# Kernel tuning notes

Hardware: AMD Instinct MI355X
Metric: run time of the kernel (lower is better)

## Reference

```python
import jax, jax.numpy as jnp
import numpy as np

B, C, G, S, R = 8192, 4096, 16, 256, 512  # batch, in_channels, clusters, cluster_size, j_rank


def setup_inputs() -> dict:
    key = jax.random.key(0)
    kx, kw, kb, kp = jax.random.split(key, 4)
    x = jax.random.normal(kx, (B, C), dtype=jnp.float32)
    # per-cluster Linear weights [G, out=R, in=S] and biases [G, R]
    W = jax.random.normal(kw, (G, R, S), dtype=jnp.float32) * (1.0 / np.sqrt(S))
    b = jax.random.normal(kb, (G, R), dtype=jnp.float32) * 0.01
    # arrangements: non-contiguous channel clusters = random permutation split into G groups
    perm = jax.random.permutation(kp, C).reshape(G, S).astype(jnp.int32)
    return {"x": x, "W": W, "b": b, "perm": perm}


def reference(x, W, b, perm):
    # gather each cluster's channels: [B, G, S]
    xg = x[:, perm]
    # batched per-cluster linear (y = x_c @ W_c^T + b_c), then concat along dim 1
    out = jnp.einsum('bgs,grs->bgr', xg, W) + b  # [B, G, R]
    return out.reshape(x.shape[0], G * R)
```

## Files before the change

### kernel.cpp

```cpp
#include <hip/hip_runtime.h>

#define BB 8192
#define CC 4096
#define GG 16
#define SS 256
#define RR 512
#define NN (GG*RR)

typedef __bf16 bf16x8 __attribute__((ext_vector_type(8)));
typedef float  f32x4_t __attribute__((ext_vector_type(4)));

__device__ __forceinline__ unsigned short f2bf(float f){
  union{float f; unsigned int u;} v; v.f = f;
  unsigned int r = (v.u + 0x7FFFu + ((v.u>>16)&1u)) >> 16;
  return (unsigned short)r;
}

__device__ __forceinline__ void gld_lds16(const void* g, void* l){
  __builtin_amdgcn_global_load_lds((const __attribute__((address_space(1))) void*)g,
                                   (__attribute__((address_space(3))) void*)l, 16, 0, 0);
}

__global__ void __launch_bounds__(256) prep_kernel(
    const float* __restrict__ x, const int* __restrict__ perm,
    const float* __restrict__ W,
    unsigned short* __restrict__ xp, unsigned short* __restrict__ Wb)
{
  __shared__ float row[CC];
  const int tid = threadIdx.x;
  const int bid = blockIdx.x;
  if (bid < BB) {
    const size_t b = bid;
    const float4* xr = (const float4*)(x + b*CC);
    float4* rr = (float4*)row;
    #pragma unroll
    for (int c=0;c<4;++c) rr[c*256+tid] = xr[c*256+tid];
    __syncthreads();
    unsigned short* xo = xp + b*CC;
    #pragma unroll
    for (int c=0;c<2;++c){
      const int j0 = (((c<<8)+tid)<<3);
      const int* pp = perm + j0;
      unsigned int w0 = (unsigned)f2bf(row[pp[0]]) | ((unsigned)f2bf(row[pp[1]])<<16);
      unsigned int w1 = (unsigned)f2bf(row[pp[2]]) | ((unsigned)f2bf(row[pp[3]])<<16);
      unsigned int w2 = (unsigned)f2bf(row[pp[4]]) | ((unsigned)f2bf(row[pp[5]])<<16);
      unsigned int w3 = (unsigned)f2bf(row[pp[6]]) | ((unsigned)f2bf(row[pp[7]])<<16);
      uint4 o; o.x=w0; o.y=w1; o.z=w2; o.w=w3;
      *(uint4*)(xo + j0) = o;
    }
  } else {
    const int i = (((bid - BB)<<8) + tid)<<3;
    float4 f0 = ((const float4*)(W+i))[0];
    float4 f1 = ((const float4*)(W+i))[1];
    uint4 o;
    o.x = (unsigned)f2bf(f0.x) | ((unsigned)f2bf(f0.y)<<16);
    o.y = (unsigned)f2bf(f0.z) | ((unsigned)f2bf(f0.w)<<16);
    o.z = (unsigned)f2bf(f1.x) | ((unsigned)f2bf(f1.y)<<16);
    o.w = (unsigned)f2bf(f1.z) | ((unsigned)f2bf(f1.w)<<16);
    *(uint4*)(Wb+i) = o;
  }
}

__global__ void __launch_bounds__(512, 4) gemm_kernel(
    const unsigned short* __restrict__ xp, const unsigned short* __restrict__ Wb,
    const float* __restrict__ bias, float* __restrict__ out)
{
  __shared__ unsigned short lA[2][128*64];
  __shared__ unsigned short lB[2][128*64];
  const int tid  = threadIdx.x;
  const int lane = tid & 63;
  const int w    = tid >> 6;
  const int wr   = w >> 2;
  const int wc   = w & 3;
  const int l15  = lane & 15, lh = lane >> 4;

  const int bid   = blockIdx.x;
  const int xcd   = bid & 7;
  const int local = bid >> 3;
  const int bx    = (xcd << 3) + (local & 7);
  const int by    = local >> 3;

  const int m0 = by << 7;
  const int n0 = bx << 7;
  const int g  = bx >> 2;
  const size_t arow0 = (size_t)m0*CC + (size_t)g*SS;
  const size_t brow0 = (size_t)n0*SS;

  f32x4_t acc[4][2];
  #pragma unroll
  for (int i=0;i<4;++i)
    #pragma unroll
    for (int j=0;j<2;++j)
      acc[i][j] = (f32x4_t){0.f,0.f,0.f,0.f};

  auto STAGE = [&](int kk, int buf){
    #pragma unroll
    for (int c=0;c<2;++c){
      const int i  = (c<<9) + tid;
      const int r  = i>>3;
      const int cs = ((i&7) ^ (r&7)) << 3;
      gld_lds16(xp + arow0 + (size_t)r*CC + kk + cs, &lA[buf][i<<3]);
    }
    #pragma unroll
    for (int c=0;c<2;++c){
      const int i  = (c<<9) + tid;
      const int r  = i>>3;
      const int cs = ((i&7) ^ (r&7)) << 3;
      gld_lds16(Wb + brow0 + (size_t)r*SS + kk + cs, &lB[buf][i<<3]);
    }
  };

  auto COMPUTE = [&](int buf){
    #pragma unroll
    for (int ks=0;ks<2;++ks){
      bf16x8 af[4], bfr[2];
      const int cc = (ks<<2) + lh;
      #pragma unroll
      for (int mi=0;mi<4;++mi){
        const int ar = (wr<<6)+(mi<<4)+l15;
        af[mi]  = *(const bf16x8*)&lA[buf][ar*64 + ((cc ^ (ar&7))<<3)];
      }
      #pragma unroll
      for (int ni=0;ni<2;++ni){
        const int br = (wc<<5)+(ni<<4)+l15;
        bfr[ni] = *(const bf16x8*)&lB[buf][br*64 + ((cc ^ (br&7))<<3)];
      }
      #pragma unroll
      for (int mi=0;mi<4;++mi)
        #pragma unroll
        for (int ni=0;ni<2;++ni)
          acc[mi][ni] = __builtin_amdgcn_mfma_f32_16x16x32_bf16(af[mi], bfr[ni], acc[mi][ni], 0,0,0);
    }
  };

  STAGE(0, 0);
  STAGE(64, 1);
  #pragma unroll
  for (int t=0;t<4;++t){
    if (t<3) asm volatile("s_waitcnt vmcnt(4)" ::: "memory");
    else     asm volatile("s_waitcnt vmcnt(0)" ::: "memory");
    __builtin_amdgcn_s_barrier();
    COMPUTE(t&1);
    __builtin_amdgcn_s_barrier();
    if (t<2) STAGE((t+2)<<6, t&1);
  }

  #pragma unroll
  for (int ni=0;ni<2;++ni){
    const int col = n0 + (wc<<5) + (ni<<4) + l15;
    const float bv = bias[col];
    #pragma unroll
    for (int mi=0;mi<4;++mi){
      const int rb = m0 + (wr<<6) + (mi<<4) + (lh<<2);
      float* op = out + (size_t)rb*NN + col;
      #pragma unroll
      for (int r=0;r<4;++r)
        op[(size_t)r*NN] = acc[mi][ni][r] + bv;
    }
  }
}

extern "C" void kernel_launch(void* const* d_in, const int* in_sizes, int n_in,
                              void* d_out, int out_size, void* d_ws, size_t ws_size,
                              hipStream_t stream) {
  const float* x    = (const float*)d_in[0];
  const float* W    = (const float*)d_in[1];
  const float* bias = (const float*)d_in[2];
  const int*   perm = (const int*)d_in[3];
  float* out = (float*)d_out;

  unsigned short* xp = (unsigned short*)d_ws;
  unsigned short* Wb = (unsigned short*)((char*)d_ws + (size_t)BB*CC*2);

  const int wblocks = (GG*RR*SS)/(256*8);
  prep_kernel<<<dim3(BB + wblocks), dim3(256), 0, stream>>>(x, perm, W, xp, Wb);
  gemm_kernel<<<dim3(4096), dim3(512), 0, stream>>>(xp, Wb, bias, out);
}
```

Measured before the change: 123.8 us.

## Pipeline prep kernel over multiple rows with async LDS loads and nontemporal stores

```diff
diff --git a/kernel.cpp b/kernel.cpp
--- a/kernel.cpp
+++ b/kernel.cpp
@@ -6,15 +6,10 @@
 #define SS 256
 #define RR 512
 #define NN (GG*RR)
+#define RPB 4
 
 typedef __bf16 bf16x8 __attribute__((ext_vector_type(8)));
 typedef float  f32x4_t __attribute__((ext_vector_type(4)));
-
-__device__ __forceinline__ unsigned short f2bf(float f){
-  union{float f; unsigned int u;} v; v.f = f;
-  unsigned int r = (v.u + 0x7FFFu + ((v.u>>16)&1u)) >> 16;
-  return (unsigned short)r;
-}
 
 __device__ __forceinline__ void gld_lds16(const void* g, void* l){
   __builtin_amdgcn_global_load_lds((const __attribute__((address_space(1))) void*)g,
@@ -26,38 +21,60 @@
     const float* __restrict__ W,
     unsigned short* __restrict__ xp, unsigned short* __restrict__ Wb)
 {
-  __shared__ float row[CC];
+  __shared__ float rows[2][CC];
   const int tid = threadIdx.x;
   const int bid = blockIdx.x;
-  if (bid < BB) {
-    const size_t b = bid;
-    const float4* xr = (const float4*)(x + b*CC);
-    float4* rr = (float4*)row;
+  if (bid < BB/RPB) {
+    const size_t b0 = (size_t)bid * RPB;
+    const int j0 = tid<<3, j1 = (256+tid)<<3;
+    const int4 pa = *(const int4*)(perm + j0);
+    const int4 pb = *(const int4*)(perm + j0 + 4);
+    const int4 pc = *(const int4*)(perm + j1);
+    const int4 pd = *(const int4*)(perm + j1 + 4);
+
+    auto STAGE = [&](int r){
+      const float* src = x + (b0+r)*CC;
+      float* dst = rows[r&1];
+      #pragma unroll
+      for (int c=0;c<4;++c){
+        const int i = (c<<8)+tid;
+        gld_lds16(src + (i<<2), dst + (i<<2));
+      }
+    };
+
+    STAGE(0);
     #pragma unroll
-    for (int c=0;c<4;++c) rr[c*256+tid] = xr[c*256+tid];
-    __syncthreads();
-    unsigned short* xo = xp + b*CC;
-    #pragma unroll
-    for (int c=0;c<2;++c){
-      const int j0 = (((c<<8)+tid)<<3);
-      const int* pp = perm + j0;
-      unsigned int w0 = (unsigned)f2bf(row[pp[0]]) | ((unsigned)f2bf(row[pp[1]])<<16);
-      unsigned int w1 = (unsigned)f2bf(row[pp[2]]) | ((unsigned)f2bf(row[pp[3]])<<16);
-      unsigned int w2 = (unsigned)f2bf(row[pp[4]]) | ((unsigned)f2bf(row[pp[5]])<<16);
-      unsigned int w3 = (unsigned)f2bf(row[pp[6]]) | ((unsigned)f2bf(row[pp[7]])<<16);
-      uint4 o; o.x=w0; o.y=w1; o.z=w2; o.w=w3;
-      *(uint4*)(xo + j0) = o;
+    for (int r=0;r<RPB;++r){
+      if (r+1<RPB){
+        STAGE(r+1);
+        asm volatile("s_waitcnt vmcnt(4)" ::: "memory");
+      } else {
+        asm volatile("s_waitcnt vmcnt(0)" ::: "memory");
+      }
+      __builtin_amdgcn_s_barrier();
+      const float* rb = rows[r&1];
+      unsigned short* xo = xp + (b0+r)*CC;
+      bf16x8 v0, v1;
+      v0[0]=(__bf16)rb[pa.x]; v0[1]=(__bf16)rb[pa.y];
+      v0[2]=(__bf16)rb[pa.z]; v0[3]=(__bf16)rb[pa.w];
+      v0[4]=(__bf16)rb[pb.x]; v0[5]=(__bf16)rb[pb.y];
+      v0[6]=(__bf16)rb[pb.z]; v0[7]=(__bf16)rb[pb.w];
+      __builtin_nontemporal_store(v0, (bf16x8*)(xo + j0));
+      v1[0]=(__bf16)rb[pc.x]; v1[1]=(__bf16)rb[pc.y];
+      v1[2]=(__bf16)rb[pc.z]; v1[3]=(__bf16)rb[pc.w];
+      v1[4]=(__bf16)rb[pd.x]; v1[5]=(__bf16)rb[pd.y];
+      v1[6]=(__bf16)rb[pd.z]; v1[7]=(__bf16)rb[pd.w];
+      __builtin_nontemporal_store(v1, (bf16x8*)(xo + j1));
+      __builtin_amdgcn_s_barrier();
     }
   } else {
-    const int i = (((bid - BB)<<8) + tid)<<3;
-    float4 f0 = ((const float4*)(W+i))[0];
-    float4 f1 = ((const float4*)(W+i))[1];
-    uint4 o;
-    o.x = (unsigned)f2bf(f0.x) | ((unsigned)f2bf(f0.y)<<16);
-    o.y = (unsigned)f2bf(f0.z) | ((unsigned)f2bf(f0.w)<<16);
-    o.z = (unsigned)f2bf(f1.x) | ((unsigned)f2bf(f1.y)<<16);
-    o.w = (unsigned)f2bf(f1.z) | ((unsigned)f2bf(f1.w)<<16);
-    *(uint4*)(Wb+i) = o;
+    const int i = (((bid - BB/RPB)<<8) + tid)<<3;
+    const float4 f0 = ((const float4*)(W+i))[0];
+    const float4 f1 = ((const float4*)(W+i))[1];
+    bf16x8 v;
+    v[0]=(__bf16)f0.x; v[1]=(__bf16)f0.y; v[2]=(__bf16)f0.z; v[3]=(__bf16)f0.w;
+    v[4]=(__bf16)f1.x; v[5]=(__bf16)f1.y; v[6]=(__bf16)f1.z; v[7]=(__bf16)f1.w;
+    __builtin_nontemporal_store(v, (bf16x8*)(Wb+i));
   }
 }
 
@@ -155,7 +172,7 @@
       float* op = out + (size_t)rb*NN + col;
       #pragma unroll
       for (int r=0;r<4;++r)
-        op[(size_t)r*NN] = acc[mi][ni][r] + bv;
+        __builtin_nontemporal_store(acc[mi][ni][r] + bv, op + (size_t)r*NN);
     }
   }
 }
@@ -173,6 +190,6 @@
   unsigned short* Wb = (unsigned short*)((char*)d_ws + (size_t)BB*CC*2);
 
   const int wblocks = (GG*RR*SS)/(256*8);
-  prep_kernel<<<dim3(BB + wblocks), dim3(256), 0, stream>>>(x, perm, W, xp, Wb);
+  prep_kernel<<<dim3(BB/RPB + wblocks), dim3(256), 0, stream>>>(x, perm, W, xp, Wb);
   gemm_kernel<<<dim3(4096), dim3(512), 0, stream>>>(xp, Wb, bias, out);
 }
```

Result: slower. 152.9 us (+23.5%).
